# Optimization experiments

Hardware: AMD Instinct MI355X
Metric: run time of the kernel (lower is better)

The kernel has to match this reference:

```python
import jax, jax.numpy as jnp
import numpy as np

D_MODEL = 1024
N_HEAD = 16
D_K = D_MODEL // N_HEAD
B, S = 2, 2048
NEG = -1000000000.0


def setup_inputs() -> dict:
    key = jax.random.key(0)
    ks = jax.random.split(key, 9)
    inp = {
        "input_q": jax.random.normal(ks[0], (B, S, D_MODEL), dtype=jnp.float32),
        "input_k": jax.random.normal(ks[1], (B, S, D_MODEL), dtype=jnp.float32),
        "input_v": jax.random.normal(ks[2], (B, S, D_MODEL), dtype=jnp.float32),
        "mask": jax.random.randint(ks[3], (1, 1, S, S), 0, 2, dtype=jnp.int32),
        # parameters (Linear weights stored as [in, out] for x @ W)
        "w_q": jax.random.normal(ks[4], (D_MODEL, D_MODEL), dtype=jnp.float32) / np.sqrt(D_MODEL),
        "w_k": jax.random.normal(ks[5], (D_MODEL, D_MODEL), dtype=jnp.float32) / np.sqrt(D_MODEL),
        "w_v": jax.random.normal(ks[6], (D_MODEL, D_MODEL), dtype=jnp.float32) / np.sqrt(D_MODEL),
        "w_o": jax.random.normal(ks[7], (D_MODEL, D_MODEL), dtype=jnp.float32) / np.sqrt(D_MODEL),
        "b_o": jax.random.normal(ks[8], (D_MODEL,), dtype=jnp.float32) * 0.01,
    }
    return inp


def reference(input_q, input_k, input_v, mask, w_q, w_k, w_v, w_o, b_o):
    b = input_q.shape[0]
    # QKV projections -> [B, H, S, d_k]
    def split_heads(x):
        return x.reshape(b, -1, N_HEAD, D_K).transpose(0, 2, 1, 3)
    q = split_heads(input_q @ w_q)
    k = split_heads(input_k @ w_k)
    v = split_heads(input_v @ w_v)
    # naive attention: materialize [B, H, Sq, Sk] scores
    scores = jnp.einsum("bhqd,bhkd->bhqk", q, k) / jnp.sqrt(jnp.float32(D_K))
    scores = jnp.where(mask == 0, jnp.float32(NEG), scores)
    attn = jax.nn.softmax(scores, axis=-1)
    per_head = jnp.einsum("bhqk,bhkd->bhqd", attn, v)
    concat = per_head.transpose(0, 2, 1, 3).reshape(b, -1, N_HEAD * D_K)
    return concat @ w_o + b_o
```

## Files before the change

### kernel.cpp

```cpp
#include <hip/hip_runtime.h>
#include <hip/hip_bf16.h>

typedef _Float16 halfx8 __attribute__((ext_vector_type(8)));
typedef _Float16 halfx4 __attribute__((ext_vector_type(4)));
typedef _Float16 half2t __attribute__((ext_vector_type(2)));
typedef __fp16 fp16x2 __attribute__((ext_vector_type(2)));
typedef float floatx4 __attribute__((ext_vector_type(4)));

constexpr int S = 2048;
constexpr int DM = 1024;
constexpr int NH = 16;
constexpr int DK = 64;
constexpr int BATCH = 2;
constexpr int MROWS = 4096;
constexpr float QSCALE = 0.125f * 1.44269504088896340736f;

#if defined(__has_builtin)
#if __has_builtin(__builtin_amdgcn_fdot2)
#define HAVE_FDOT2 1
#endif
#if __has_builtin(__builtin_amdgcn_exp2f)
#define EXP2F(x) __builtin_amdgcn_exp2f(x)
#endif
#endif
#ifndef EXP2F
#define EXP2F(x) __builtin_exp2f(x)
#endif

static __device__ inline half2t pack2(float a, float b) {
  return __builtin_bit_cast(half2t, __builtin_amdgcn_cvt_pkrtz(a, b));
}

static __device__ inline float hdot2(half2t a, half2t b, float c) {
#ifdef HAVE_FDOT2
  return __builtin_amdgcn_fdot2(__builtin_bit_cast(fp16x2, a),
                                __builtin_bit_cast(fp16x2, b), c, false);
#else
  return c + (float)a[0] * (float)b[0] + (float)a[1] * (float)b[1];
#endif
}

static __device__ inline void load_lds16(const _Float16* g, _Float16* l) {
  __builtin_amdgcn_global_load_lds((const __attribute__((address_space(1))) void*)g,
                                   (__attribute__((address_space(3))) void*)l, 16, 0, 0);
}

__global__ __launch_bounds__(256) void prep(const float* __restrict__ w_q,
                                            const float* __restrict__ w_k,
                                            const float* __restrict__ w_v,
                                            const float* __restrict__ w_o,
                                            _Float16* __restrict__ wqkv,
                                            _Float16* __restrict__ wto,
                                            const float* __restrict__ in_q,
                                            const float* __restrict__ in_k,
                                            const float* __restrict__ in_v,
                                            _Float16* __restrict__ xq,
                                            _Float16* __restrict__ xk,
                                            _Float16* __restrict__ xv,
                                            const int* __restrict__ mask,
                                            _Float16* __restrict__ Mt) {
  __shared__ float tile[32][33];
  const int bid = blockIdx.x;
  const int tid = threadIdx.x;
  if (bid < 4096) {
    int wsel = bid >> 10, t = bid & 1023;
    const float* w = (wsel == 0) ? w_q : (wsel == 1) ? w_k : (wsel == 2) ? w_v : w_o;
    _Float16* wt = (wsel < 3) ? (wqkv + (size_t)wsel * DM * DM) : wto;
    int n0 = (t & 31) * 32, k0 = (t >> 5) * 32;
    int tx = tid & 31, ty = tid >> 5;
#pragma unroll
    for (int i = 0; i < 4; ++i)
      tile[ty + i * 8][tx] = w[(size_t)(k0 + ty + i * 8) * DM + n0 + tx];
    __syncthreads();
#pragma unroll
    for (int i = 0; i < 4; ++i)
      wt[(size_t)(n0 + ty + i * 8) * DM + k0 + tx] = (_Float16)tile[tx][ty + i * 8];
  } else if (bid < 10240) {
    int idx = bid - 4096, isel = idx >> 11, blk = idx & 2047;
    const float* a = (isel == 0) ? in_q : (isel == 1) ? in_k : in_v;
    _Float16* o = (isel == 0) ? xq : (isel == 1) ? xk : xv;
    size_t i = ((size_t)blk * 256 + tid) * 8;
    float4 va = *(const float4*)(a + i);
    float4 vb = *(const float4*)(a + i + 4);
    union { halfx8 v; _Float16 h[8]; } u;
    u.h[0] = (_Float16)va.x; u.h[1] = (_Float16)va.y;
    u.h[2] = (_Float16)va.z; u.h[3] = (_Float16)va.w;
    u.h[4] = (_Float16)vb.x; u.h[5] = (_Float16)vb.y;
    u.h[6] = (_Float16)vb.z; u.h[7] = (_Float16)vb.w;
    *(halfx8*)(o + i) = u.v;
  } else {
    int t = (bid - 10240) * 256 + tid;
    int j0 = (t & 1) * 8;
    int quad = (t >> 1) & 3;
    int q = (t >> 3) & (S - 1);
    int kt = t >> 14;
    const int* src = mask + (size_t)q * S + kt * 64 + (j0 >> 2) * 16 + quad * 4;
    int4 a = *(const int4*)src;
    int4 b = *(const int4*)(src + 16);
    union { halfx8 v; _Float16 h[8]; } u;
    u.h[0] = (_Float16)(a.x != 0); u.h[1] = (_Float16)(a.y != 0);
    u.h[2] = (_Float16)(a.z != 0); u.h[3] = (_Float16)(a.w != 0);
    u.h[4] = (_Float16)(b.x != 0); u.h[5] = (_Float16)(b.y != 0);
    u.h[6] = (_Float16)(b.z != 0); u.h[7] = (_Float16)(b.w != 0);
    *(halfx8*)(Mt + (size_t)t * 8) = u.v;
  }
}

__global__ __launch_bounds__(256) void qkv_gemm(const _Float16* __restrict__ xq,
                                                const _Float16* __restrict__ xk,
                                                const _Float16* __restrict__ xv,
                                                const _Float16* __restrict__ wqkv,
                                                _Float16* __restrict__ Qf,
                                                _Float16* __restrict__ Kf,
                                                _Float16* __restrict__ Vt) {
  __shared__ __align__(16) _Float16 smem[17408];
  _Float16* Asm = smem;
  _Float16* Bsm = smem + 128 * 64;
  const int tid = threadIdx.x;
  const int w = tid >> 6, l = tid & 63, lo = l & 15, quad = l >> 4;
  const int lo7 = l & 7;
  const int wm = (w >> 1) * 64, wn = (w & 1) * 64;
  const int bx = blockIdx.x, bm = blockIdx.y * 128;
  const int wid = bx >> 3;
  const _Float16* A = (wid == 0) ? xq : (wid == 1) ? xk : xv;
  const _Float16* Bt = wqkv + (size_t)bx * 128 * DM;

  floatx4 acc[4][4] = {};

  for (int k0 = 0; k0 < DM; k0 += 64) {
#pragma unroll
    for (int i = 0; i < 4; ++i) {
      int chunk = i * 256 + tid;
      int r = chunk >> 3;
      int c = (chunk & 7) ^ (r & 7);
      load_lds16(A + (size_t)(bm + r) * DM + k0 + c * 8, Asm + chunk * 8);
    }
#pragma unroll
    for (int i = 0; i < 4; ++i) {
      int chunk = i * 256 + tid;
      int r = chunk >> 3;
      int c = (chunk & 7) ^ (r & 7);
      load_lds16(Bt + (size_t)r * DM + k0 + c * 8, Bsm + chunk * 8);
    }
    __syncthreads();

#pragma unroll
    for (int ks = 0; ks < 2; ++ks) {
      halfx8 af[4], bf[4];
#pragma unroll
      for (int mt = 0; mt < 4; ++mt)
        af[mt] = *(const halfx8*)&Asm[(wm + mt * 16 + lo) * 64 + (((ks * 4 + quad) ^ lo7) * 8)];
#pragma unroll
      for (int nt = 0; nt < 4; ++nt)
        bf[nt] = *(const halfx8*)&Bsm[(wn + nt * 16 + lo) * 64 + (((ks * 4 + quad) ^ lo7) * 8)];
#pragma unroll
      for (int mt = 0; mt < 4; ++mt)
#pragma unroll
        for (int nt = 0; nt < 4; ++nt)
          acc[mt][nt] =
              __builtin_amdgcn_mfma_f32_16x16x32_f16(af[mt], bf[nt], acc[mt][nt], 0, 0, 0);
    }
    __syncthreads();
  }

  if (wid == 2) {
    constexpr int LDTT = 136;
    _Float16* tb = smem;
#pragma unroll
    for (int mt = 0; mt < 4; ++mt)
#pragma unroll
      for (int nt = 0; nt < 4; ++nt)
#pragma unroll
        for (int r = 0; r < 4; ++r) {
          int dl = wn + nt * 16 + lo;
          int sl = wm + mt * 16 + quad * 4 + r;
          tb[dl * LDTT + sl] = (_Float16)acc[mt][nt][r];
        }
    __syncthreads();
    const int b = bm >> 11, s0 = bm & (S - 1);
    const int d2 = tid >> 1, chunk = (tid & 1) * 64;
    const int dg = ((bx & 7) * 128 + d2);
    const int h = dg >> 6, dd = dg & 63;
    _Float16* O = Vt + ((size_t)(b * NH + h) * DK + dd) * S + s0 + chunk;
#pragma unroll
    for (int j = 0; j < 8; ++j)
      *(halfx8*)(O + j * 8) = *(const halfx8*)&tb[d2 * LDTT + chunk + j * 8];
    return;
  }

  _Float16* Out = (wid == 0) ? Qf : Kf;
  const float scale = (wid == 0) ? QSCALE : 1.0f;
#pragma unroll
  for (int mt = 0; mt < 4; ++mt)
#pragma unroll
    for (int nt = 0; nt < 4; ++nt)
#pragma unroll
      for (int r = 0; r < 4; ++r) {
        int row = bm + wm + mt * 16 + quad * 4 + r;
        int col = (bx & 7) * 128 + wn + nt * 16 + lo;
        Out[(size_t)row * DM + col] = (_Float16)(acc[mt][nt][r] * scale);
      }
}

__global__ __launch_bounds__(128, 2) void attn_kernel(const _Float16* __restrict__ Qf,
                                                      const _Float16* __restrict__ Kf,
                                                      const _Float16* __restrict__ Vt,
                                                      const _Float16* __restrict__ Mt,
                                                      _Float16* __restrict__ concat) {
  __shared__ __align__(16) _Float16 K0s[64 * 64], K1s[64 * 64];
  __shared__ __align__(16) _Float16 V0s[64 * 64], V1s[64 * 64];
  __shared__ __align__(16) _Float16 Psm[2 * 32 * 64];

  const int tid = threadIdx.x;
  const int w = tid >> 6, l = tid & 63, lo = l & 15, quad = l >> 4, lo7 = l & 7;
  const int qb = blockIdx.x * 64 + w * 32;
  const int h = blockIdx.y, b = blockIdx.z;

  const _Float16* Kbase = Kf + (size_t)b * S * DM + h * DK;
  const _Float16* Vb = Vt + (size_t)(b * NH + h) * DK * S;
  _Float16* Pw = Psm + w * 32 * 64;

  halfx8 qf[2][2];
  const _Float16* Mp[2];
#pragma unroll
  for (int g = 0; g < 2; ++g) {
#pragma unroll
    for (int ks = 0; ks < 2; ++ks)
      qf[g][ks] = *(const halfx8*)(Qf + ((size_t)b * S + qb + g * 16 + lo) * DM + h * DK +
                                   ks * 32 + quad * 8);
    Mp[g] = Mt + ((size_t)(qb + g * 16 + lo) * 4 + quad) * 16;
  }

  floatx4 Oacc[2][4] = {};
  float lsum[2] = {0.f, 0.f};
  const half2t onev = {(_Float16)1.0f, (_Float16)1.0f};

  auto stage = [&](int kt, _Float16* Kd, _Float16* Vd) {
#pragma unroll
    for (int i = 0; i < 4; ++i) {
      int chunk = i * 128 + tid;
      int r = chunk >> 3;
      int c = (chunk & 7) ^ (r & 7);
      load_lds16(Kbase + (size_t)(kt * 64 + r) * DM + c * 8, Kd + chunk * 8);
      load_lds16(Vb + (size_t)r * S + kt * 64 + c * 8, Vd + chunk * 8);
    }
  };

  auto tile = [&](const _Float16* Kc, const _Float16* Vc, const halfx8* mc) {
    floatx4 Sacc[2][4] = {};
#pragma unroll
    for (int ks = 0; ks < 2; ++ks)
#pragma unroll
      for (int nt = 0; nt < 4; ++nt) {
        halfx8 kf = *(const halfx8*)&Kc[(nt * 16 + lo) * 64 + (((ks * 4 + quad) ^ lo7) * 8)];
        Sacc[0][nt] = __builtin_amdgcn_mfma_f32_16x16x32_f16(kf, qf[0][ks], Sacc[0][nt], 0, 0, 0);
        Sacc[1][nt] = __builtin_amdgcn_mfma_f32_16x16x32_f16(kf, qf[1][ks], Sacc[1][nt], 0, 0, 0);
      }
#pragma unroll
    for (int g = 0; g < 2; ++g) {
      union { halfx8 v; half2t h2[4]; } mu0, mu1;
      mu0.v = mc[g * 2];
      mu1.v = mc[g * 2 + 1];
      half2t mm[8] = {mu0.h2[0], mu0.h2[1], mu0.h2[2], mu0.h2[3],
                      mu1.h2[0], mu1.h2[1], mu1.h2[2], mu1.h2[3]};
#pragma unroll
      for (int nt = 0; nt < 4; ++nt) {
        half2t p01 = pack2(EXP2F(Sacc[g][nt][0]), EXP2F(Sacc[g][nt][1]));
        half2t p23 = pack2(EXP2F(Sacc[g][nt][2]), EXP2F(Sacc[g][nt][3]));
        p01 *= mm[nt * 2];
        p23 *= mm[nt * 2 + 1];
        lsum[g] = hdot2(p01, onev, lsum[g]);
        lsum[g] = hdot2(p23, onev, lsum[g]);
        union { halfx4 v; half2t hh[2]; } u;
        u.hh[0] = p01;
        u.hh[1] = p23;
        *(halfx4*)&Pw[(g * 16 + lo) * 64 + (((2 * nt + (quad >> 1)) ^ lo7) * 8) +
                      (quad & 1) * 4] = u.v;
      }
    }
#pragma unroll
    for (int ks = 0; ks < 2; ++ks) {
      halfx8 pf0 = *(const halfx8*)&Pw[lo * 64 + (((ks * 4 + quad) ^ lo7) * 8)];
      halfx8 pf1 = *(const halfx8*)&Pw[(16 + lo) * 64 + (((ks * 4 + quad) ^ lo7) * 8)];
#pragma unroll
      for (int nt = 0; nt < 4; ++nt) {
        halfx8 vf = *(const halfx8*)&Vc[(nt * 16 + lo) * 64 + (((ks * 4 + quad) ^ lo7) * 8)];
        Oacc[0][nt] = __builtin_amdgcn_mfma_f32_16x16x32_f16(pf0, vf, Oacc[0][nt], 0, 0, 0);
        Oacc[1][nt] = __builtin_amdgcn_mfma_f32_16x16x32_f16(pf1, vf, Oacc[1][nt], 0, 0, 0);
      }
    }
  };

  halfx8 mr[4];
#pragma unroll
  for (int g = 0; g < 2; ++g) {
    mr[g * 2] = *(const halfx8*)(Mp[g]);
    mr[g * 2 + 1] = *(const halfx8*)(Mp[g] + 8);
  }
  stage(0, K0s, V0s);

  for (int kt = 0; kt < S / 64; kt += 2) {
    __syncthreads();
    stage(kt + 1, K1s, V1s);
    halfx8 mc[4] = {mr[0], mr[1], mr[2], mr[3]};
#pragma unroll
    for (int g = 0; g < 2; ++g) {
      mr[g * 2] = *(const halfx8*)(Mp[g] + (size_t)(kt + 1) * 131072);
      mr[g * 2 + 1] = *(const halfx8*)(Mp[g] + (size_t)(kt + 1) * 131072 + 8);
    }
    tile(K0s, V0s, mc);
    __syncthreads();
    if (kt + 2 < S / 64) stage(kt + 2, K0s, V0s);
    mc[0] = mr[0]; mc[1] = mr[1]; mc[2] = mr[2]; mc[3] = mr[3];
    if (kt + 2 < S / 64) {
#pragma unroll
      for (int g = 0; g < 2; ++g) {
        mr[g * 2] = *(const halfx8*)(Mp[g] + (size_t)(kt + 2) * 131072);
        mr[g * 2 + 1] = *(const halfx8*)(Mp[g] + (size_t)(kt + 2) * 131072 + 8);
      }
    }
    tile(K1s, V1s, mc);
  }

#pragma unroll
  for (int g = 0; g < 2; ++g) {
    lsum[g] += __shfl_xor(lsum[g], 16);
    lsum[g] += __shfl_xor(lsum[g], 32);
  }

#pragma unroll
  for (int g = 0; g < 2; ++g)
#pragma unroll
    for (int r = 0; r < 4; ++r) {
      float lr = __shfl(lsum[g], quad * 4 + r);
      float inv = __builtin_amdgcn_rcpf(lr);
      int q = qb + g * 16 + quad * 4 + r;
#pragma unroll
      for (int nt = 0; nt < 4; ++nt) {
        int d = nt * 16 + lo;
        concat[((size_t)b * S + q) * DM + h * DK + d] = (_Float16)(Oacc[g][nt][r] * inv);
      }
    }
}

__global__ __launch_bounds__(256) void out_gemm(const _Float16* __restrict__ A,
                                                const _Float16* __restrict__ Bt,
                                                float* __restrict__ Cp,
                                                const float* __restrict__ bias) {
  __shared__ __align__(16) _Float16 A0s[128 * 64], A1s[128 * 64];
  __shared__ __align__(16) _Float16 B0s[64 * 64], B1s[64 * 64];
  const int tid = threadIdx.x;
  const int w = tid >> 6, l = tid & 63, lo = l & 15, quad = l >> 4, lo7 = l & 7;
  const int wm = (w >> 1) * 64, wn = (w & 1) * 32;
  const int bm = blockIdx.y * 128, bn = blockIdx.x * 64;

  floatx4 acc[4][2] = {};

  auto stageg = [&](int k0, _Float16* Ad, _Float16* Bd) {
#pragma unroll
    for (int i = 0; i < 4; ++i) {
      int chunk = i * 256 + tid;
      int rr = chunk >> 3;
      int cc = (chunk & 7) ^ (rr & 7);
      load_lds16(A + (size_t)(bm + rr) * DM + k0 + cc * 8, Ad + chunk * 8);
    }
#pragma unroll
    for (int i = 0; i < 2; ++i) {
      int chunk = i * 256 + tid;
      int rr = chunk >> 3;
      int cc = (chunk & 7) ^ (rr & 7);
      load_lds16(Bt + (size_t)(bn + rr) * DM + k0 + cc * 8, Bd + chunk * 8);
    }
  };
  auto comp = [&](const _Float16* As, const _Float16* Bs) {
#pragma unroll
    for (int ks = 0; ks < 2; ++ks) {
      halfx8 af[4], bf[2];
#pragma unroll
      for (int mt = 0; mt < 4; ++mt)
        af[mt] = *(const halfx8*)&As[(wm + mt * 16 + lo) * 64 + (((ks * 4 + quad) ^ lo7) * 8)];
#pragma unroll
      for (int nt = 0; nt < 2; ++nt)
        bf[nt] = *(const halfx8*)&Bs[(wn + nt * 16 + lo) * 64 + (((ks * 4 + quad) ^ lo7) * 8)];
#pragma unroll
      for (int mt = 0; mt < 4; ++mt)
#pragma unroll
        for (int nt = 0; nt < 2; ++nt)
          acc[mt][nt] =
              __builtin_amdgcn_mfma_f32_16x16x32_f16(af[mt], bf[nt], acc[mt][nt], 0, 0, 0);
    }
  };

  stageg(0, A0s, B0s);
  for (int k0 = 0; k0 < DM; k0 += 128) {
    __syncthreads();
    stageg(k0 + 64, A1s, B1s);
    comp(A0s, B0s);
    __syncthreads();
    if (k0 + 128 < DM) stageg(k0 + 128, A0s, B0s);
    comp(A1s, B1s);
  }

  float bv[2];
#pragma unroll
  for (int nt = 0; nt < 2; ++nt) bv[nt] = bias[bn + wn + nt * 16 + lo];
#pragma unroll
  for (int mt = 0; mt < 4; ++mt)
#pragma unroll
    for (int nt = 0; nt < 2; ++nt)
#pragma unroll
      for (int r = 0; r < 4; ++r) {
        int row = bm + wm + mt * 16 + quad * 4 + r;
        int col = bn + wn + nt * 16 + lo;
        Cp[(size_t)row * DM + col] = acc[mt][nt][r] + bv[nt];
      }
}

extern "C" void kernel_launch(void* const* d_in, const int* in_sizes, int n_in,
                              void* d_out, int out_size, void* d_ws, size_t ws_size,
                              hipStream_t stream) {
  const float* in_q = (const float*)d_in[0];
  const float* in_k = (const float*)d_in[1];
  const float* in_v = (const float*)d_in[2];
  const int* mask = (const int*)d_in[3];
  const float* w_q = (const float*)d_in[4];
  const float* w_k = (const float*)d_in[5];
  const float* w_v = (const float*)d_in[6];
  const float* w_o = (const float*)d_in[7];
  const float* b_o = (const float*)d_in[8];
  float* out = (float*)d_out;

  char* ws = (char*)d_ws;
  constexpr size_t WB = (size_t)DM * DM * sizeof(_Float16);
  constexpr size_t MB_ = (size_t)S * S * sizeof(_Float16);
  constexpr size_t TB = (size_t)MROWS * DM * sizeof(_Float16);
  _Float16* wqkv = (_Float16*)(ws);
  _Float16* wto = (_Float16*)(ws + 3 * WB);
  _Float16* Mt = (_Float16*)(ws + 4 * WB);
  char* p = ws + 4 * WB + MB_;
  _Float16* Qf = (_Float16*)(p);
  _Float16* Kf = (_Float16*)(p + TB);
  _Float16* Vt = (_Float16*)(p + 2 * TB);
  _Float16* xq = (_Float16*)(p + 3 * TB);
  _Float16* xk = (_Float16*)(p + 4 * TB);
  _Float16* xv = (_Float16*)(p + 5 * TB);
  _Float16* concat = xq;

  prep<<<dim3(12288), 256, 0, stream>>>(w_q, w_k, w_v, w_o, wqkv, wto,
                                        in_q, in_k, in_v, xq, xk, xv, mask, Mt);
  qkv_gemm<<<dim3(24, 32), 256, 0, stream>>>(xq, xk, xv, wqkv, Qf, Kf, Vt);
  attn_kernel<<<dim3(S / 64, NH, BATCH), 128, 0, stream>>>(Qf, Kf, Vt, Mt, concat);
  out_gemm<<<dim3(DM / 64, MROWS / 128), 256, 0, stream>>>(concat, wto, out, b_o);
}
```

Baseline: 245.7 us.

## Split attention along the key dimension into two halves and add a combine kernel

The attention kernel now processes half of the key sequence per block, which doubles the grid. It also shrinks the K/V tiles from 64 to 32 keys and raises the occupancy hint to 4 blocks per CU. Each half writes unnormalized fp16 partial outputs plus row sums, and a new combine kernel adds the two halves and normalizes them into concat. This is meant to raise parallelism and occupancy for the 1024-block grid, at the cost of extra global traffic for the partials and an additional launch. Because no max subtraction is used, the unscaled partial sums are written and added in fp16, which risks overflow or precision loss.

```diff
diff --git a/kernel.cpp b/kernel.cpp
--- a/kernel.cpp
+++ b/kernel.cpp
@@ -202,23 +202,26 @@
       }
 }
 
-__global__ __launch_bounds__(128, 2) void attn_kernel(const _Float16* __restrict__ Qf,
+__global__ __launch_bounds__(128, 4) void attn_kernel(const _Float16* __restrict__ Qf,
                                                       const _Float16* __restrict__ Kf,
                                                       const _Float16* __restrict__ Vt,
                                                       const _Float16* __restrict__ Mt,
-                                                      _Float16* __restrict__ concat) {
-  __shared__ __align__(16) _Float16 K0s[64 * 64], K1s[64 * 64];
-  __shared__ __align__(16) _Float16 V0s[64 * 64], V1s[64 * 64];
-  __shared__ __align__(16) _Float16 Psm[2 * 32 * 64];
+                                                      _Float16* __restrict__ Opart,
+                                                      float* __restrict__ lpart) {
+  __shared__ __align__(16) _Float16 K0s[32 * 64], K1s[32 * 64];
+  __shared__ __align__(16) _Float16 V0s[64 * 32], V1s[64 * 32];
+  __shared__ __align__(16) _Float16 Psm[2 * 32 * 32];
 
   const int tid = threadIdx.x;
-  const int w = tid >> 6, l = tid & 63, lo = l & 15, quad = l >> 4, lo7 = l & 7;
+  const int w = tid >> 6, l = tid & 63, lo = l & 15, quad = l >> 4;
+  const int lo7 = l & 7, lo3 = l & 3;
   const int qb = blockIdx.x * 64 + w * 32;
-  const int h = blockIdx.y, b = blockIdx.z;
-
-  const _Float16* Kbase = Kf + (size_t)b * S * DM + h * DK;
-  const _Float16* Vb = Vt + (size_t)(b * NH + h) * DK * S;
-  _Float16* Pw = Psm + w * 32 * 64;
+  const int h = blockIdx.y, zz = blockIdx.z;
+  const int b = zz >> 1, ks2 = zz & 1;
+
+  const _Float16* Kbase = Kf + ((size_t)b * S + ks2 * 1024) * DM + h * DK;
+  const _Float16* Vb = Vt + (size_t)(b * NH + h) * DK * S + ks2 * 1024;
+  _Float16* Pw = Psm + w * 32 * 32;
 
   halfx8 qf[2][2];
   const _Float16* Mp[2];
@@ -237,88 +240,78 @@
 
   auto stage = [&](int kt, _Float16* Kd, _Float16* Vd) {
 #pragma unroll
-    for (int i = 0; i < 4; ++i) {
-      int chunk = i * 128 + tid;
-      int r = chunk >> 3;
-      int c = (chunk & 7) ^ (r & 7);
-      load_lds16(Kbase + (size_t)(kt * 64 + r) * DM + c * 8, Kd + chunk * 8);
-      load_lds16(Vb + (size_t)r * S + kt * 64 + c * 8, Vd + chunk * 8);
+    for (int i = 0; i < 2; ++i) {
+      int ch = i * 128 + tid;
+      int r = ch >> 3, c = (ch & 7) ^ (r & 7);
+      load_lds16(Kbase + (size_t)(kt * 32 + r) * DM + c * 8, Kd + ch * 8);
+    }
+#pragma unroll
+    for (int i = 0; i < 2; ++i) {
+      int ch = i * 128 + tid;
+      int r = ch >> 2, c = (ch & 3) ^ (r & 3);
+      load_lds16(Vb + (size_t)r * S + kt * 32 + c * 8, Vd + ch * 8);
     }
   };
 
   auto tile = [&](const _Float16* Kc, const _Float16* Vc, const halfx8* mc) {
-    floatx4 Sacc[2][4] = {};
+    floatx4 Sacc[2][2] = {};
 #pragma unroll
     for (int ks = 0; ks < 2; ++ks)
 #pragma unroll
-      for (int nt = 0; nt < 4; ++nt) {
+      for (int nt = 0; nt < 2; ++nt) {
         halfx8 kf = *(const halfx8*)&Kc[(nt * 16 + lo) * 64 + (((ks * 4 + quad) ^ lo7) * 8)];
         Sacc[0][nt] = __builtin_amdgcn_mfma_f32_16x16x32_f16(kf, qf[0][ks], Sacc[0][nt], 0, 0, 0);
         Sacc[1][nt] = __builtin_amdgcn_mfma_f32_16x16x32_f16(kf, qf[1][ks], Sacc[1][nt], 0, 0, 0);
       }
 #pragma unroll
     for (int g = 0; g < 2; ++g) {
-      union { halfx8 v; half2t h2[4]; } mu0, mu1;
-      mu0.v = mc[g * 2];
-      mu1.v = mc[g * 2 + 1];
-      half2t mm[8] = {mu0.h2[0], mu0.h2[1], mu0.h2[2], mu0.h2[3],
-                      mu1.h2[0], mu1.h2[1], mu1.h2[2], mu1.h2[3]};
-#pragma unroll
-      for (int nt = 0; nt < 4; ++nt) {
+      union { halfx8 v; half2t h2[4]; } mu;
+      mu.v = mc[g];
+#pragma unroll
+      for (int nt = 0; nt < 2; ++nt) {
         half2t p01 = pack2(EXP2F(Sacc[g][nt][0]), EXP2F(Sacc[g][nt][1]));
         half2t p23 = pack2(EXP2F(Sacc[g][nt][2]), EXP2F(Sacc[g][nt][3]));
-        p01 *= mm[nt * 2];
-        p23 *= mm[nt * 2 + 1];
+        p01 *= mu.h2[nt * 2];
+        p23 *= mu.h2[nt * 2 + 1];
         lsum[g] = hdot2(p01, onev, lsum[g]);
         lsum[g] = hdot2(p23, onev, lsum[g]);
         union { halfx4 v; half2t hh[2]; } u;
         u.hh[0] = p01;
         u.hh[1] = p23;
-        *(halfx4*)&Pw[(g * 16 + lo) * 64 + (((2 * nt + (quad >> 1)) ^ lo7) * 8) +
+        *(halfx4*)&Pw[(g * 16 + lo) * 32 + (((2 * nt + (quad >> 1)) ^ lo3) * 8) +
                       (quad & 1) * 4] = u.v;
       }
     }
-#pragma unroll
-    for (int ks = 0; ks < 2; ++ks) {
-      halfx8 pf0 = *(const halfx8*)&Pw[lo * 64 + (((ks * 4 + quad) ^ lo7) * 8)];
-      halfx8 pf1 = *(const halfx8*)&Pw[(16 + lo) * 64 + (((ks * 4 + quad) ^ lo7) * 8)];
-#pragma unroll
-      for (int nt = 0; nt < 4; ++nt) {
-        halfx8 vf = *(const halfx8*)&Vc[(nt * 16 + lo) * 64 + (((ks * 4 + quad) ^ lo7) * 8)];
-        Oacc[0][nt] = __builtin_amdgcn_mfma_f32_16x16x32_f16(pf0, vf, Oacc[0][nt], 0, 0, 0);
-        Oacc[1][nt] = __builtin_amdgcn_mfma_f32_16x16x32_f16(pf1, vf, Oacc[1][nt], 0, 0, 0);
-      }
+    halfx8 pf0 = *(const halfx8*)&Pw[lo * 32 + ((quad ^ lo3) * 8)];
+    halfx8 pf1 = *(const halfx8*)&Pw[(16 + lo) * 32 + ((quad ^ lo3) * 8)];
+#pragma unroll
+    for (int nt = 0; nt < 4; ++nt) {
+      halfx8 vf = *(const halfx8*)&Vc[(nt * 16 + lo) * 32 + ((quad ^ lo3) * 8)];
+      Oacc[0][nt] = __builtin_amdgcn_mfma_f32_16x16x32_f16(pf0, vf, Oacc[0][nt], 0, 0, 0);
+      Oacc[1][nt] = __builtin_amdgcn_mfma_f32_16x16x32_f16(pf1, vf, Oacc[1][nt], 0, 0, 0);
     }
   };
 
-  halfx8 mr[4];
-#pragma unroll
-  for (int g = 0; g < 2; ++g) {
-    mr[g * 2] = *(const halfx8*)(Mp[g]);
-    mr[g * 2 + 1] = *(const halfx8*)(Mp[g] + 8);
-  }
+  auto mload = [&](int kt, halfx8* dst) {
+    size_t off = (size_t)(ks2 * 16 + (kt >> 1)) * 131072 + (kt & 1) * 8;
+#pragma unroll
+    for (int g = 0; g < 2; ++g) dst[g] = *(const halfx8*)(Mp[g] + off);
+  };
+
+  halfx8 mr[2];
+  mload(0, mr);
   stage(0, K0s, V0s);
 
-  for (int kt = 0; kt < S / 64; kt += 2) {
+  for (int kt = 0; kt < 32; kt += 2) {
     __syncthreads();
     stage(kt + 1, K1s, V1s);
-    halfx8 mc[4] = {mr[0], mr[1], mr[2], mr[3]};
-#pragma unroll
-    for (int g = 0; g < 2; ++g) {
-      mr[g * 2] = *(const halfx8*)(Mp[g] + (size_t)(kt + 1) * 131072);
-      mr[g * 2 + 1] = *(const halfx8*)(Mp[g] + (size_t)(kt + 1) * 131072 + 8);
-    }
+    halfx8 mc[2] = {mr[0], mr[1]};
+    mload(kt + 1, mr);
     tile(K0s, V0s, mc);
     __syncthreads();
-    if (kt + 2 < S / 64) stage(kt + 2, K0s, V0s);
-    mc[0] = mr[0]; mc[1] = mr[1]; mc[2] = mr[2]; mc[3] = mr[3];
-    if (kt + 2 < S / 64) {
-#pragma unroll
-      for (int g = 0; g < 2; ++g) {
-        mr[g * 2] = *(const halfx8*)(Mp[g] + (size_t)(kt + 2) * 131072);
-        mr[g * 2 + 1] = *(const halfx8*)(Mp[g] + (size_t)(kt + 2) * 131072 + 8);
-      }
-    }
+    if (kt + 2 < 32) stage(kt + 2, K0s, V0s);
+    mc[0] = mr[0]; mc[1] = mr[1];
+    if (kt + 2 < 32) mload(kt + 2, mr);
     tile(K1s, V1s, mc);
   }
 
@@ -328,19 +321,40 @@
     lsum[g] += __shfl_xor(lsum[g], 32);
   }
 
-#pragma unroll
-  for (int g = 0; g < 2; ++g)
+  _Float16* Ob = Opart + (size_t)ks2 * MROWS * DM;
+#pragma unroll
+  for (int g = 0; g < 2; ++g) {
 #pragma unroll
     for (int r = 0; r < 4; ++r) {
-      float lr = __shfl(lsum[g], quad * 4 + r);
-      float inv = __builtin_amdgcn_rcpf(lr);
       int q = qb + g * 16 + quad * 4 + r;
 #pragma unroll
       for (int nt = 0; nt < 4; ++nt) {
         int d = nt * 16 + lo;
-        concat[((size_t)b * S + q) * DM + h * DK + d] = (_Float16)(Oacc[g][nt][r] * inv);
+        Ob[((size_t)b * S + q) * DM + h * DK + d] = (_Float16)Oacc[g][nt][r];
       }
     }
+    if (l < 16)
+      lpart[(size_t)ks2 * BATCH * NH * S + (size_t)(b * NH + h) * S + qb + g * 16 + l] =
+          lsum[g];
+  }
+}
+
+__global__ __launch_bounds__(256) void combine(const _Float16* __restrict__ Opart,
+                                               const float* __restrict__ lpart,
+                                               _Float16* __restrict__ concat) {
+  size_t i = ((size_t)blockIdx.x * 256 + threadIdx.x) * 8;
+  int row = (int)(i >> 10), col = (int)(i & 1023);
+  int b = row >> 11, s = row & (S - 1), h = col >> 6;
+  float lt = lpart[(size_t)(b * NH + h) * S + s] +
+             lpart[(size_t)BATCH * NH * S + (size_t)(b * NH + h) * S + s];
+  float inv = __builtin_amdgcn_rcpf(lt);
+  halfx8 a = *(const halfx8*)(Opart + i);
+  halfx8 c = *(const halfx8*)(Opart + (size_t)MROWS * DM + i);
+  union { halfx8 v; _Float16 hh[8]; } u;
+#pragma unroll
+  for (int j = 0; j < 8; ++j)
+    u.hh[j] = (_Float16)(((float)a[j] + (float)c[j]) * inv);
+  *(halfx8*)(concat + i) = u.v;
 }
 
 __global__ __launch_bounds__(256) void out_gemm(const _Float16* __restrict__ A,
@@ -444,11 +458,14 @@
   _Float16* xq = (_Float16*)(p + 3 * TB);
   _Float16* xk = (_Float16*)(p + 4 * TB);
   _Float16* xv = (_Float16*)(p + 5 * TB);
-  _Float16* concat = xq;
+  _Float16* Opart = xq;
+  _Float16* concat = xv;
+  float* lpart = (float*)wqkv;
 
   prep<<<dim3(12288), 256, 0, stream>>>(w_q, w_k, w_v, w_o, wqkv, wto,
                                         in_q, in_k, in_v, xq, xk, xv, mask, Mt);
   qkv_gemm<<<dim3(24, 32), 256, 0, stream>>>(xq, xk, xv, wqkv, Qf, Kf, Vt);
-  attn_kernel<<<dim3(S / 64, NH, BATCH), 128, 0, stream>>>(Qf, Kf, Vt, Mt, concat);
+  attn_kernel<<<dim3(S / 64, NH, BATCH * 2), 128, 0, stream>>>(Qf, Kf, Vt, Mt, Opart, lpart);
+  combine<<<dim3(MROWS * DM / 8 / 256), 256, 0, stream>>>(Opart, lpart, concat);
   out_gemm<<<dim3(DM / 64, MROWS / 128), 256, 0, stream>>>(concat, wto, out, b_o);
 }
```

New measurement: 260.2 us. +5.9%, slower.
